# Kernel optimization log

Measured on AMD Instinct MI355X. Metric: run time of the kernel, lower is better.

Reference implementation:

```python
import jax, jax.numpy as jnp
import numpy as np
from jax import lax

B, N = 8, 107136          # batch, anchors (248*216*2)
SCORE_THRESH = 0.05
PRE_MAX = 2048            # nms_pre_max_sizes[0]
POST_MAX = 128            # nms_post_max_sizes[0]
IOU_THRESH = 0.5
NUM_DIR_BINS = 2
DIR_OFFSET = 0.0
POST_CENTER_RANGE = np.array([0.0, -39.68, -5.0, 69.12, 39.68, 5.0], np.float32)


def setup_inputs() -> dict:
    key = jax.random.key(0)
    k1, k2, k3, k4, k5 = jax.random.split(key, 5)
    box_preds = jax.random.normal(k1, (B, N, 7), jnp.float32) * 0.3
    cls_preds = jax.random.normal(k2, (B, N, 2), jnp.float32) * 2.0
    dir_preds = jax.random.normal(k3, (B, N, 2), jnp.float32)
    # realistic KITTI car anchors: (x, y, z, w, l, h, r)
    xs = jax.random.uniform(k4, (B, N), jnp.float32, 0.0, 69.12)
    ys = jax.random.uniform(k5, (B, N), jnp.float32, -39.68, 39.68)
    zs = jnp.full((B, N), -1.0, jnp.float32)
    w = jnp.full((B, N), 1.6, jnp.float32)
    l = jnp.full((B, N), 3.9, jnp.float32)
    h = jnp.full((B, N), 1.56, jnp.float32)
    r = jnp.broadcast_to(jnp.where(jnp.arange(N) % 2 == 0, 0.0, np.pi / 2).astype(jnp.float32), (B, N))
    anchors = jnp.stack([xs, ys, zs, w, l, h, r], axis=-1)
    return {"box_preds": box_preds, "cls_preds": cls_preds, "dir_preds": dir_preds, "anchors": anchors}


def _decode(bp, an):
    # GroundBox3dCoder.decode_torch (second/pointpillars), code order (x,y,z,w,l,h,r)
    xa, ya, za, wa, la, ha, ra = [an[..., i] for i in range(7)]
    xt, yt, zt, wt, lt, ht, rt = [bp[..., i] for i in range(7)]
    za = za + ha * 0.5
    diag = jnp.sqrt(la * la + wa * wa)
    xg = xt * diag + xa
    yg = yt * diag + ya
    zg = zt * ha + za
    lg = jnp.exp(lt) * la
    wg = jnp.exp(wt) * wa
    hg = jnp.exp(ht) * ha
    rg = rt + ra
    zg = zg - hg * 0.5
    return jnp.stack([xg, yg, zg, wg, lg, hg, rg], axis=-1)


def _standup(boxes):
    # boxes: [K,7] decoded; rotated 2d rect -> axis-aligned standup box (x1,y1,x2,y2)
    x, y, w, l, r = boxes[:, 0], boxes[:, 1], boxes[:, 3], boxes[:, 4], boxes[:, 6]
    c, s = jnp.abs(jnp.cos(r)), jnp.abs(jnp.sin(r))
    hx = 0.5 * (w * c + l * s)
    hy = 0.5 * (w * s + l * c)
    return jnp.stack([x - hx, y - hy, x + hx, y + hy], axis=-1)


def _pairwise_iou(bb):
    # bb: [K,4] standup boxes
    x1, y1, x2, y2 = bb[:, 0], bb[:, 1], bb[:, 2], bb[:, 3]
    area = (x2 - x1) * (y2 - y1)
    ix = jnp.maximum(0.0, jnp.minimum(x2[:, None], x2[None, :]) - jnp.maximum(x1[:, None], x1[None, :]))
    iy = jnp.maximum(0.0, jnp.minimum(y2[:, None], y2[None, :]) - jnp.maximum(y1[:, None], y1[None, :]))
    inter = ix * iy
    return inter / jnp.maximum(area[:, None] + area[None, :] - inter, 1e-8)


def _greedy_nms(ious, valid):
    K = valid.shape[0]
    idxs = jnp.arange(K)
    def body(i, keep):
        sup = (ious[i] > IOU_THRESH) & (idxs > i) & keep[i]
        return keep & ~sup
    return lax.fori_loop(0, K, body, valid)


def _limit_period(val, offset, period):
    return val - jnp.floor(val / period + offset) * period


def _predict_one(boxes, scores, dir_labels):
    # boxes [N,7], scores [N], dir_labels [N] int32 (already sorted? no: raw)
    masked = jnp.where(scores >= SCORE_THRESH, scores, -jnp.inf)
    top_s, idx = lax.top_k(masked, PRE_MAX)           # sorted desc
    b = boxes[idx]                                    # [K,7]
    dl = dir_labels[idx]
    valid = jnp.isfinite(top_s)
    ious = _pairwise_iou(_standup(b))
    keep = _greedy_nms(lax.stop_gradient(ious), valid)
    kept = jnp.where(keep, top_s, -jnp.inf)
    sel_s, sel_i = lax.top_k(kept, POST_MAX)
    sel_b = b[sel_i]
    sel_dl = dl[sel_i].astype(sel_b.dtype)
    period = 2.0 * np.pi / NUM_DIR_BINS
    dir_rot = _limit_period(sel_b[:, 6] - DIR_OFFSET, 0.0, period)
    new_r = dir_rot + DIR_OFFSET + period * sel_dl
    sel_b = jnp.concatenate([sel_b[:, :6], new_r[:, None]], axis=-1)
    pcr = jnp.asarray(POST_CENTER_RANGE)
    in_range = jnp.all(sel_b[:, :3] >= pcr[:3], axis=1) & jnp.all(sel_b[:, :3] <= pcr[3:], axis=1)
    mask = jnp.isfinite(sel_s) & in_range
    out_s = jnp.where(mask, sel_s, 0.0)
    out_b = jnp.where(mask[:, None], sel_b, 0.0)
    labels = jnp.zeros((POST_MAX,), jnp.int32)  # single fg class -> label 0
    return out_b, out_s, labels, mask


def reference(box_preds, cls_preds, dir_preds, anchors):
    decoded = _decode(box_preds, anchors)                    # [B,N,7]
    scores = jax.nn.softmax(cls_preds, axis=-1)[..., 1]      # [B,N]
    dir_labels = jnp.argmax(dir_preds, axis=-1).astype(jnp.int32)
    return jax.vmap(_predict_one)(decoded, scores, dir_labels)
```

## Files before the change

### kernel.cpp

```cpp
#include <hip/hip_runtime.h>
#include <stdint.h>

#define NB 8
#define NN 107136
#define TOTAL (NB * NN)
#define NPAIR (NN / 2)
#define PRE 2048
#define POST 128
#define CAP 4096
#define HBINS 128
#define KEYBASE 0xBF00u
#define SCORE_TH 0.05f
#define SH_BPB 53

static constexpr size_t OFF_SCORES = 0;
static constexpr size_t SZ_SCORES  = (size_t)TOTAL * 4;
static constexpr size_t OFF_HIST   = OFF_SCORES + SZ_SCORES;
static constexpr size_t SZ_HIST    = (size_t)NB * SH_BPB * HBINS * 4;
static constexpr size_t OFF_CNT    = OFF_HIST + SZ_HIST;
static constexpr size_t SZ_CNT     = (size_t)NB * 64 * 4;
static constexpr size_t OFF_CAND   = OFF_CNT + SZ_CNT + 256;
static constexpr size_t SZ_CAND    = (size_t)NB * CAP * 8;
static constexpr size_t OFF_SELS   = OFF_CAND + SZ_CAND;
static constexpr size_t OFF_SELI   = OFF_SELS + (size_t)NB * PRE * 4;
static constexpr size_t OFF_SELB   = OFF_SELI + (size_t)NB * PRE * 4;
static constexpr size_t OFF_SBB    = OFF_SELB + (size_t)NB * PRE * 7 * 4;
static constexpr size_t OFF_SAR    = OFF_SBB + (size_t)NB * PRE * 4 * 4;


__global__ void __launch_bounds__(256) k_scoreshist(const float* __restrict__ cls,
                                                    float* __restrict__ scores,
                                                    uint32_t* __restrict__ hp,
                                                    uint32_t* __restrict__ counts,
                                                    uint64_t* __restrict__ cand) {
    int b = blockIdx.y;
    int t = threadIdx.x;
    if (blockIdx.x == 0 && t == 0) counts[(size_t)b * 64] = 0u;
    if (blockIdx.x < 16)
        cand[(size_t)b * CAP + blockIdx.x * 256 + t] = 0ull;
    __shared__ uint32_t lh[HBINS];
    if (t < HBINS) lh[t] = 0u;
    __syncthreads();
    const float4* cp = (const float4*)cls + (size_t)b * NPAIR;
    float2* sp = (float2*)scores + (size_t)b * NPAIR;
#pragma unroll
    for (int k = 0; k < 4; k++) {
        int p = blockIdx.x * 1024 + k * 256 + t;
        if (p < NPAIR) {
            float4 c = cp[p];
            float m0 = fmaxf(c.x, c.y);
            float s0 = __fdiv_rn(expf(__fsub_rn(c.y, m0)),
                                 __fadd_rn(expf(__fsub_rn(c.x, m0)), expf(__fsub_rn(c.y, m0))));
            float m1 = fmaxf(c.z, c.w);
            float s1 = __fdiv_rn(expf(__fsub_rn(c.w, m1)),
                                 __fadd_rn(expf(__fsub_rn(c.z, m1)), expf(__fsub_rn(c.w, m1))));
            sp[p] = make_float2(s0, s1);
            if (s0 >= 0.5f) {
                uint32_t bin = ((__float_as_uint(s0) >> 16) | 0x8000u) - KEYBASE;
                if (bin > 127u) bin = 127u;
                atomicAdd(&lh[bin], 1u);
            }
            if (s1 >= 0.5f) {
                uint32_t bin = ((__float_as_uint(s1) >> 16) | 0x8000u) - KEYBASE;
                if (bin > 127u) bin = 127u;
                atomicAdd(&lh[bin], 1u);
            }
        }
    }
    __syncthreads();
    if (t < HBINS) hp[((size_t)b * SH_BPB + blockIdx.x) * HBINS + t] = lh[t];
}

__global__ void __launch_bounds__(256) k_compact(const float* __restrict__ scores,
                                                 const uint32_t* __restrict__ hp,
                                                 uint32_t* __restrict__ counts,
                                                 uint64_t* __restrict__ cand) {
    int g2 = blockIdx.x * 256 + threadIdx.x;
    int lane = threadIdx.x & 63, wid = threadIdx.x >> 6;
    int e0 = 2 * g2;
    int b = e0 / NN;

    uint32_t h0 = 0, h1 = 0;
    const uint32_t* hb = hp + (size_t)b * SH_BPB * HBINS;
#pragma unroll 4
    for (int sg = 0; sg < SH_BPB; sg++) {
        h0 += hb[sg * HBINS + 2 * lane];
        h1 += hb[sg * HBINS + 2 * lane + 1];
    }
    uint32_t v = h0 + h1;
    for (int off = 1; off < 64; off <<= 1) {
        uint32_t u = __shfl_down(v, off);
        if (lane + off >= 64) u = 0u;
        v += u;
    }
    uint32_t total = __shfl(v, 0);
    int c = -1;
    if (v - h0 >= PRE) c = 2 * lane + 1;
    else if (v >= PRE) c = 2 * lane;
    for (int off = 32; off > 0; off >>= 1) c = max(c, __shfl_xor(c, off));
    uint32_t Tb = (total >= PRE && c >= 0) ? (KEYBASE + (uint32_t)c) : 0u;

    float2 sv = ((const float2*)scores)[g2];
    uint32_t key0 = __float_as_uint(sv.x) | 0x80000000u;
    uint32_t key1 = __float_as_uint(sv.y) | 0x80000000u;
    bool p0 = (sv.x >= SCORE_TH) && ((key0 >> 16) >= Tb);
    bool p1 = (sv.y >= SCORE_TH) && ((key1 >> 16) >= Tb);
    uint64_t bal0 = __ballot(p0), bal1 = __ballot(p1);
    uint32_t n0 = (uint32_t)__popcll(bal0);
    uint32_t wcnt = n0 + (uint32_t)__popcll(bal1);
    uint64_t below = (1ull << lane) - 1ull;
    uint32_t off0 = (uint32_t)__popcll(bal0 & below);
    uint32_t off1 = n0 + (uint32_t)__popcll(bal1 & below);
    __shared__ uint32_t lcnt[2];
    __shared__ uint32_t gbase[2];
    __shared__ uint32_t wbase[4];
    int b0 = (blockIdx.x * 512) / NN;
    if (threadIdx.x < 2) lcnt[threadIdx.x] = 0u;
    __syncthreads();
    if (lane == 0 && wcnt) wbase[wid] = atomicAdd(&lcnt[b - b0], wcnt);
    __syncthreads();
    if (threadIdx.x < 2 && lcnt[threadIdx.x])
        gbase[threadIdx.x] = atomicAdd(&counts[(size_t)(b0 + threadIdx.x) * 64], lcnt[threadIdx.x]);
    __syncthreads();
    if (p0 | p1) {
        uint32_t base = gbase[b - b0] + wbase[wid];
        if (p0) {
            uint32_t slot = base + off0;
            if (slot < CAP)
                cand[(size_t)b * CAP + slot] =
                    ((uint64_t)key0 << 32) | (uint64_t)(0xFFFFFFFFu - (uint32_t)(e0 - b * NN));
        }
        if (p1) {
            uint32_t slot = base + off1;
            if (slot < CAP)
                cand[(size_t)b * CAP + slot] =
                    ((uint64_t)key1 << 32) | (uint64_t)(0xFFFFFFFFu - (uint32_t)(e0 + 1 - b * NN));
        }
    }
}

__global__ void __launch_bounds__(256) k_rank_decode(
        const uint64_t* __restrict__ cand, const uint32_t* __restrict__ counts,
        const float* __restrict__ box_preds, const float* __restrict__ anchors,
        float* __restrict__ selS, uint32_t* __restrict__ selI,
        float* __restrict__ selB, float* __restrict__ selBB, float* __restrict__ selA) {
    int b = blockIdx.y;
    int m = (int)counts[(size_t)b * 64]; if (m > CAP) m = CAP;
    int i0 = blockIdx.x * 256;
    if (i0 >= m) return;
    int t = threadIdx.x;
    int i = i0 + t;
    const uint64_t* cb = cand + (size_t)b * CAP;
    uint64_t mykey = (i < m) ? cb[i] : ~0ull;
    __shared__ uint64_t tile[512];
    uint32_t rank = 0;
    int ntiles = (m + 511) >> 9;
    for (int tt = 0; tt < ntiles; tt++) {
        int base = tt << 9;
        tile[t] = cb[base + t];
        tile[t + 256] = cb[base + 256 + t];
        __syncthreads();
#pragma unroll 16
        for (int j = 0; j < 512; j++)
            rank += (tile[j] > mykey) ? 1u : 0u;
        __syncthreads();
    }
    if (i >= m || rank >= PRE) return;

    size_t o = (size_t)b * PRE + rank;
    uint32_t key = (uint32_t)(mykey >> 32);
    uint32_t idx = 0xFFFFFFFFu - (uint32_t)(mykey & 0xFFFFFFFFull);
    float score = __uint_as_float(key & 0x7FFFFFFFu);
    const float* bp = box_preds + ((size_t)b * NN + idx) * 7;
    const float* an = anchors + ((size_t)b * NN + idx) * 7;
    float xa = an[0], ya = an[1], za = an[2], wa = an[3], la = an[4], ha = an[5], ra = an[6];
    float xt = bp[0], yt = bp[1], zt = bp[2], wt = bp[3], lt = bp[4], ht = bp[5], rt = bp[6];
    float za2  = __fadd_rn(za, __fmul_rn(ha, 0.5f));
    float diag = sqrtf(__fadd_rn(__fmul_rn(la, la), __fmul_rn(wa, wa)));
    float xg = __fadd_rn(__fmul_rn(xt, diag), xa);
    float yg = __fadd_rn(__fmul_rn(yt, diag), ya);
    float zg = __fadd_rn(__fmul_rn(zt, ha), za2);
    float lg = __fmul_rn(expf(lt), la);
    float wg = __fmul_rn(expf(wt), wa);
    float hg = __fmul_rn(expf(ht), ha);
    float rg = __fadd_rn(rt, ra);
    zg = __fsub_rn(zg, __fmul_rn(hg, 0.5f));
    selS[o] = score; selI[o] = idx;
    selB[o * 7 + 0] = xg; selB[o * 7 + 1] = yg; selB[o * 7 + 2] = zg;
    selB[o * 7 + 3] = wg; selB[o * 7 + 4] = lg; selB[o * 7 + 5] = hg;
    selB[o * 7 + 6] = rg;
    float cc = fabsf(cosf(rg)), ss = fabsf(sinf(rg));
    float hx = __fmul_rn(0.5f, __fadd_rn(__fmul_rn(wg, cc), __fmul_rn(lg, ss)));
    float hy = __fmul_rn(0.5f, __fadd_rn(__fmul_rn(wg, ss), __fmul_rn(lg, cc)));
    float x1 = __fsub_rn(xg, hx), y1 = __fsub_rn(yg, hy);
    float x2 = __fadd_rn(xg, hx), y2 = __fadd_rn(yg, hy);
    selBB[o * 4 + 0] = x1; selBB[o * 4 + 1] = y1;
    selBB[o * 4 + 2] = x2; selBB[o * 4 + 3] = y2;
    selA[o] = __fmul_rn(__fsub_rn(x2, x1), __fsub_rn(y2, y1));
}

__global__ void __launch_bounds__(128) k_nms(
        const float* __restrict__ selBB, const float* __restrict__ selA,
        const float* __restrict__ selS, const uint32_t* __restrict__ selI,
        const float* __restrict__ selB, const uint32_t* __restrict__ counts,
        const float* __restrict__ dir_preds, float* __restrict__ out) {
    int b = blockIdx.x;
    int t = threadIdx.x;
    __shared__ float4 sbb[PRE];
    __shared__ float  sar[PRE];
    __shared__ int keptIdx[POST];
    __shared__ int keptCountSh;
    int Mv = (int)counts[(size_t)b * 64]; if (Mv > PRE) Mv = PRE;
    const float4* bb4 = (const float4*)selBB + (size_t)b * PRE;
    const float*  ar  = selA + (size_t)b * PRE;
    for (int i = t; i < PRE; i += 128) {
        sbb[i] = bb4[i];
        sar[i] = ar[i];
    }
    __syncthreads();
    if (t < 64) {
        int lane = t;
        float ax1 = 1e30f, ay1 = 1e30f, ax2 = 1e30f, ay2 = 1e30f, aar = 0.f;
        float bx1 = 1e30f, by1 = 1e30f, bx2 = 1e30f, by2 = 1e30f, bar = 0.f;
        int kc = 0;
        for (int i = 0; i < Mv && kc < POST; i++) {
            float4 c = sbb[i];
            float ca = sar[i];
            float ix = fmaxf(0.f, __fsub_rn(fminf(ax2, c.z), fmaxf(ax1, c.x)));
            float iy = fmaxf(0.f, __fsub_rn(fminf(ay2, c.w), fmaxf(ay1, c.y)));
            float inter = __fmul_rn(ix, iy);
            float den = fmaxf(__fsub_rn(__fadd_rn(aar, ca), inter), 1e-8f);
            bool sup = inter > __fmul_rn(0.5f, den);
            ix = fmaxf(0.f, __fsub_rn(fminf(bx2, c.z), fmaxf(bx1, c.x)));
            iy = fmaxf(0.f, __fsub_rn(fminf(by2, c.w), fmaxf(by1, c.y)));
            inter = __fmul_rn(ix, iy);
            den = fmaxf(__fsub_rn(__fadd_rn(bar, ca), inter), 1e-8f);
            sup = sup || (inter > __fmul_rn(0.5f, den));
            if (__ballot(sup) == 0ull) {
                if (lane == 0) keptIdx[kc] = i;
                if (kc < 64) {
                    if (lane == kc) { ax1 = c.x; ay1 = c.y; ax2 = c.z; ay2 = c.w; aar = ca; }
                } else {
                    if (lane == kc - 64) { bx1 = c.x; by1 = c.y; bx2 = c.z; by2 = c.w; bar = ca; }
                }
                kc++;
            }
        }
        if (lane == 0) keptCountSh = kc;
    }
    __syncthreads();
    int kc = keptCountSh;
    size_t ob = (size_t)b * POST + t;
    float box[7] = {0.f, 0.f, 0.f, 0.f, 0.f, 0.f, 0.f};
    float sc = 0.f, mk = 0.f;
    if (t < kc) {
        int i = keptIdx[t];
        size_t o = (size_t)b * PRE + i;
        float s = selS[o];
        uint32_t idx = selI[o];
        const float* bx = selB + o * 7;
        float d0 = dir_preds[((size_t)b * NN + idx) * 2 + 0];
        float d1 = dir_preds[((size_t)b * NN + idx) * 2 + 1];
        float label = (d1 > d0) ? 1.0f : 0.0f;
        const float period = 3.14159265358979323846f;
        float r = bx[6];
        float dir_rot = __fsub_rn(r, __fmul_rn(floorf(__fdiv_rn(r, period)), period));
        float nr = __fadd_rn(dir_rot, __fmul_rn(period, label));
        float x = bx[0], y = bx[1], z = bx[2];
        bool in_range = (x >= 0.0f) && (y >= -39.68f) && (z >= -5.0f) &&
                        (x <= 69.12f) && (y <= 39.68f) && (z <= 5.0f);
        if (in_range) {
            box[0] = x; box[1] = y; box[2] = z;
            box[3] = bx[3]; box[4] = bx[4]; box[5] = bx[5]; box[6] = nr;
            sc = s; mk = 1.f;
        }
    }
    float* out_b = out;
    float* out_s = out + 7168;
    float* out_l = out + 8192;
    float* out_m = out + 9216;
    for (int c = 0; c < 7; c++) out_b[ob * 7 + c] = box[c];
    out_s[ob] = sc;
    out_l[ob] = 0.f;
    out_m[ob] = mk;
}

extern "C" void kernel_launch(void* const* d_in, const int* in_sizes, int n_in,
                              void* d_out, int out_size, void* d_ws, size_t ws_size,
                              hipStream_t stream) {
    const float* box_preds = (const float*)d_in[0];
    const float* cls_preds = (const float*)d_in[1];
    const float* dir_preds = (const float*)d_in[2];
    const float* anchors   = (const float*)d_in[3];
    float* out = (float*)d_out;
    char* ws = (char*)d_ws;

    float*    scores = (float*)(ws + OFF_SCORES);
    uint32_t* hp     = (uint32_t*)(ws + OFF_HIST);
    uint32_t* counts = (uint32_t*)(ws + OFF_CNT);
    uint64_t* cand   = (uint64_t*)(ws + OFF_CAND);
    float*    selS   = (float*)(ws + OFF_SELS);
    uint32_t* selI   = (uint32_t*)(ws + OFF_SELI);
    float*    selB   = (float*)(ws + OFF_SELB);
    float*    selBB  = (float*)(ws + OFF_SBB);
    float*    selA   = (float*)(ws + OFF_SAR);

    dim3 gSH(SH_BPB, NB);
    k_scoreshist<<<gSH, 256, 0, stream>>>(cls_preds, scores, hp, counts, cand);
    k_compact<<<TOTAL / 512, 256, 0, stream>>>(scores, hp, counts, cand);
    dim3 gRank(CAP / 256, NB);
    k_rank_decode<<<gRank, 256, 0, stream>>>(cand, counts, box_preds, anchors,
                                             selS, selI, selB, selBB, selA);
    k_nms<<<NB, 128, 0, stream>>>(selBB, selA, selS, selI, selB, counts,
                                  dir_preds, out);
}
```

Baseline: 178.0 us.

## Fuse four pipeline kernels into one cooperative persistent kernel with grid syncs

Replaces the four separate launches (score/histogram, compaction, rank+decode, NMS) with a single cooperative kernel of 256 blocks that separates the phases with grid.sync. Each block computes all per-batch thresholds redundantly and loops over several compaction chunks. The aim is to remove launch overhead and the gaps between dependent kernels. In exchange it adds grid-wide barrier costs, repeated threshold work in every block, and a final serial NMS phase that runs on only 8 blocks while the rest sit idle.

```diff
diff --git a/kernel.cpp b/kernel.cpp
--- a/kernel.cpp
+++ b/kernel.cpp
@@ -1,22 +1,29 @@
 #include <hip/hip_runtime.h>
+#include <hip/hip_cooperative_groups.h>
 #include <stdint.h>
+
+namespace cg = cooperative_groups;
 
 #define NB 8
 #define NN 107136
 #define TOTAL (NB * NN)
 #define NPAIR (NN / 2)
+#define NPAIRS_ALL (TOTAL / 2)
 #define PRE 2048
 #define POST 128
 #define CAP 4096
 #define HBINS 128
 #define KEYBASE 0xBF00u
 #define SCORE_TH 0.05f
-#define SH_BPB 53
+#define NSEG 32
+#define SEGP (NPAIR / NSEG)
+#define NBLK 256
+#define NTHR 256
 
 static constexpr size_t OFF_SCORES = 0;
 static constexpr size_t SZ_SCORES  = (size_t)TOTAL * 4;
 static constexpr size_t OFF_HIST   = OFF_SCORES + SZ_SCORES;
-static constexpr size_t SZ_HIST    = (size_t)NB * SH_BPB * HBINS * 4;
+static constexpr size_t SZ_HIST    = (size_t)NB * NSEG * HBINS * 4;
 static constexpr size_t OFF_CNT    = OFF_HIST + SZ_HIST;
 static constexpr size_t SZ_CNT     = (size_t)NB * 64 * 4;
 static constexpr size_t OFF_CAND   = OFF_CNT + SZ_CNT + 256;
@@ -27,262 +34,274 @@
 static constexpr size_t OFF_SBB    = OFF_SELB + (size_t)NB * PRE * 7 * 4;
 static constexpr size_t OFF_SAR    = OFF_SBB + (size_t)NB * PRE * 4 * 4;
 
-
-__global__ void __launch_bounds__(256) k_scoreshist(const float* __restrict__ cls,
-                                                    float* __restrict__ scores,
-                                                    uint32_t* __restrict__ hp,
-                                                    uint32_t* __restrict__ counts,
-                                                    uint64_t* __restrict__ cand) {
-    int b = blockIdx.y;
+#define SM_BYTES 41600
+
+__global__ void __launch_bounds__(256) k_mega(
+        const float* __restrict__ box_preds, const float* __restrict__ cls,
+        const float* __restrict__ dir_preds, const float* __restrict__ anchors,
+        float* scores, uint32_t* hp, uint32_t* counts, uint64_t* cand,
+        float* selS, uint32_t* selI, float* selB, float* selBB, float* selA,
+        float* out) {
+    cg::grid_group grid = cg::this_grid();
+    __shared__ __align__(16) unsigned char smraw[SM_BYTES];
     int t = threadIdx.x;
-    if (blockIdx.x == 0 && t == 0) counts[(size_t)b * 64] = 0u;
-    if (blockIdx.x < 16)
-        cand[(size_t)b * CAP + blockIdx.x * 256 + t] = 0ull;
-    __shared__ uint32_t lh[HBINS];
-    if (t < HBINS) lh[t] = 0u;
-    __syncthreads();
-    const float4* cp = (const float4*)cls + (size_t)b * NPAIR;
-    float2* sp = (float2*)scores + (size_t)b * NPAIR;
+    int blk = blockIdx.x;
+    int lane = t & 63, wid = t >> 6;
+
+    {
+        uint32_t* lh = (uint32_t*)smraw;
+        int b = blk >> 5, seg = blk & 31;
+        if (blk < NB && t == 0) counts[(size_t)blk * 64] = 0u;
+        if (t < 128) cand[(size_t)blk * 128 + t] = 0ull;
+        if (t < HBINS) lh[t] = 0u;
+        __syncthreads();
+        const float4* cp = (const float4*)cls + (size_t)b * NPAIR;
+        float2* sp = (float2*)scores + (size_t)b * NPAIR;
+        int base = seg * SEGP;
 #pragma unroll
-    for (int k = 0; k < 4; k++) {
-        int p = blockIdx.x * 1024 + k * 256 + t;
-        if (p < NPAIR) {
-            float4 c = cp[p];
-            float m0 = fmaxf(c.x, c.y);
-            float s0 = __fdiv_rn(expf(__fsub_rn(c.y, m0)),
-                                 __fadd_rn(expf(__fsub_rn(c.x, m0)), expf(__fsub_rn(c.y, m0))));
-            float m1 = fmaxf(c.z, c.w);
-            float s1 = __fdiv_rn(expf(__fsub_rn(c.w, m1)),
-                                 __fadd_rn(expf(__fsub_rn(c.z, m1)), expf(__fsub_rn(c.w, m1))));
-            sp[p] = make_float2(s0, s1);
-            if (s0 >= 0.5f) {
-                uint32_t bin = ((__float_as_uint(s0) >> 16) | 0x8000u) - KEYBASE;
-                if (bin > 127u) bin = 127u;
-                atomicAdd(&lh[bin], 1u);
-            }
-            if (s1 >= 0.5f) {
-                uint32_t bin = ((__float_as_uint(s1) >> 16) | 0x8000u) - KEYBASE;
-                if (bin > 127u) bin = 127u;
-                atomicAdd(&lh[bin], 1u);
-            }
-        }
+        for (int k = 0; k < 7; k++) {
+            int pl = k * 256 + t;
+            if (pl < SEGP) {
+                int p = base + pl;
+                float4 c = cp[p];
+                float m0 = fmaxf(c.x, c.y);
+                float s0 = __fdiv_rn(expf(__fsub_rn(c.y, m0)),
+                                     __fadd_rn(expf(__fsub_rn(c.x, m0)), expf(__fsub_rn(c.y, m0))));
+                float m1 = fmaxf(c.z, c.w);
+                float s1 = __fdiv_rn(expf(__fsub_rn(c.w, m1)),
+                                     __fadd_rn(expf(__fsub_rn(c.z, m1)), expf(__fsub_rn(c.w, m1))));
+                sp[p] = make_float2(s0, s1);
+                if (s0 >= 0.5f) {
+                    uint32_t bin = ((__float_as_uint(s0) >> 16) | 0x8000u) - KEYBASE;
+                    if (bin > 127u) bin = 127u;
+                    atomicAdd(&lh[bin], 1u);
+                }
+                if (s1 >= 0.5f) {
+                    uint32_t bin = ((__float_as_uint(s1) >> 16) | 0x8000u) - KEYBASE;
+                    if (bin > 127u) bin = 127u;
+                    atomicAdd(&lh[bin], 1u);
+                }
+            }
+        }
+        __syncthreads();
+        if (t < HBINS) hp[((size_t)(b * NSEG + seg)) * HBINS + t] = lh[t];
     }
-    __syncthreads();
-    if (t < HBINS) hp[((size_t)b * SH_BPB + blockIdx.x) * HBINS + t] = lh[t];
-}
-
-__global__ void __launch_bounds__(256) k_compact(const float* __restrict__ scores,
-                                                 const uint32_t* __restrict__ hp,
-                                                 uint32_t* __restrict__ counts,
-                                                 uint64_t* __restrict__ cand) {
-    int g2 = blockIdx.x * 256 + threadIdx.x;
-    int lane = threadIdx.x & 63, wid = threadIdx.x >> 6;
-    int e0 = 2 * g2;
-    int b = e0 / NN;
-
-    uint32_t h0 = 0, h1 = 0;
-    const uint32_t* hb = hp + (size_t)b * SH_BPB * HBINS;
+    __threadfence();
+    grid.sync();
+
+    {
+        struct P2S { uint32_t sT[8]; uint32_t lcnt[2]; uint32_t gbase[2]; uint32_t wbase[4]; };
+        P2S* s2 = (P2S*)smraw;
+        for (int bb = wid; bb < NB; bb += 4) {
+            uint32_t h0 = 0, h1 = 0;
+            const uint32_t* hb = hp + (size_t)bb * NSEG * HBINS;
 #pragma unroll 4
-    for (int sg = 0; sg < SH_BPB; sg++) {
-        h0 += hb[sg * HBINS + 2 * lane];
-        h1 += hb[sg * HBINS + 2 * lane + 1];
+            for (int sg = 0; sg < NSEG; sg++) {
+                h0 += hb[sg * HBINS + 2 * lane];
+                h1 += hb[sg * HBINS + 2 * lane + 1];
+            }
+            uint32_t v = h0 + h1;
+            for (int off = 1; off < 64; off <<= 1) {
+                uint32_t u = __shfl_down(v, off);
+                if (lane + off >= 64) u = 0u;
+                v += u;
+            }
+            uint32_t total = __shfl(v, 0);
+            int c = -1;
+            if (v - h0 >= PRE) c = 2 * lane + 1;
+            else if (v >= PRE) c = 2 * lane;
+            for (int off = 32; off > 0; off >>= 1) c = max(c, __shfl_xor(c, off));
+            if (lane == 0) s2->sT[bb] = (total >= PRE && c >= 0) ? (KEYBASE + (uint32_t)c) : 0u;
+        }
+        __syncthreads();
+        for (int it = 0; it < 7; it++) {
+            int g2 = it * 65536 + blk * 256 + t;
+            bool valid = g2 < NPAIRS_ALL;
+            int g2c = valid ? g2 : NPAIRS_ALL - 1;
+            int e0 = 2 * g2c;
+            int b = e0 / NN;
+            uint32_t Tb = s2->sT[b];
+            float2 sv = make_float2(0.f, 0.f);
+            if (valid) sv = ((const float2*)scores)[g2c];
+            uint32_t key0 = __float_as_uint(sv.x) | 0x80000000u;
+            uint32_t key1 = __float_as_uint(sv.y) | 0x80000000u;
+            bool p0 = valid && (sv.x >= SCORE_TH) && ((key0 >> 16) >= Tb);
+            bool p1 = valid && (sv.y >= SCORE_TH) && ((key1 >> 16) >= Tb);
+            uint64_t bal0 = __ballot(p0), bal1 = __ballot(p1);
+            uint32_t n0 = (uint32_t)__popcll(bal0);
+            uint32_t wcnt = n0 + (uint32_t)__popcll(bal1);
+            uint64_t below = (1ull << lane) - 1ull;
+            uint32_t off0 = (uint32_t)__popcll(bal0 & below);
+            uint32_t off1 = n0 + (uint32_t)__popcll(bal1 & below);
+            int b0 = (it * 131072 + blk * 512) / NN;
+            __syncthreads();
+            if (t < 2) s2->lcnt[t] = 0u;
+            __syncthreads();
+            if (lane == 0 && wcnt) s2->wbase[wid] = atomicAdd(&s2->lcnt[b - b0], wcnt);
+            __syncthreads();
+            if (t < 2 && s2->lcnt[t])
+                s2->gbase[t] = atomicAdd(&counts[(size_t)(b0 + t) * 64], s2->lcnt[t]);
+            __syncthreads();
+            if (p0 | p1) {
+                uint32_t base = s2->gbase[b - b0] + s2->wbase[wid];
+                if (p0) {
+                    uint32_t slot = base + off0;
+                    if (slot < CAP)
+                        cand[(size_t)b * CAP + slot] =
+                            ((uint64_t)key0 << 32) | (uint64_t)(0xFFFFFFFFu - (uint32_t)(e0 - b * NN));
+                }
+                if (p1) {
+                    uint32_t slot = base + off1;
+                    if (slot < CAP)
+                        cand[(size_t)b * CAP + slot] =
+                            ((uint64_t)key1 << 32) | (uint64_t)(0xFFFFFFFFu - (uint32_t)(e0 + 1 - b * NN));
+                }
+            }
+        }
     }
-    uint32_t v = h0 + h1;
-    for (int off = 1; off < 64; off <<= 1) {
-        uint32_t u = __shfl_down(v, off);
-        if (lane + off >= 64) u = 0u;
-        v += u;
+    __threadfence();
+    grid.sync();
+
+    {
+        uint64_t* tile = (uint64_t*)smraw;
+        int b = blk >> 5, k = blk & 31;
+        int m = (int)counts[(size_t)b * 64]; if (m > CAP) m = CAP;
+        int i0 = k * 256;
+        bool active = (k < 16) && (i0 < m);
+        if (active) {
+            int i = i0 + t;
+            const uint64_t* cb = cand + (size_t)b * CAP;
+            uint64_t mykey = (i < m) ? cb[i] : ~0ull;
+            uint32_t rank = 0;
+            int ntiles = (m + 511) >> 9;
+            for (int tt = 0; tt < ntiles; tt++) {
+                int base = tt << 9;
+                tile[t] = cb[base + t];
+                tile[t + 256] = cb[base + 256 + t];
+                __syncthreads();
+#pragma unroll 16
+                for (int j = 0; j < 512; j++)
+                    rank += (tile[j] > mykey) ? 1u : 0u;
+                __syncthreads();
+            }
+            if (i < m && rank < PRE) {
+                size_t o = (size_t)b * PRE + rank;
+                uint32_t key = (uint32_t)(mykey >> 32);
+                uint32_t idx = 0xFFFFFFFFu - (uint32_t)(mykey & 0xFFFFFFFFull);
+                float score = __uint_as_float(key & 0x7FFFFFFFu);
+                const float* bp = box_preds + ((size_t)b * NN + idx) * 7;
+                const float* an = anchors + ((size_t)b * NN + idx) * 7;
+                float xa = an[0], ya = an[1], za = an[2], wa = an[3], la = an[4], ha = an[5], ra = an[6];
+                float xt = bp[0], yt = bp[1], zt = bp[2], wt = bp[3], lt = bp[4], ht = bp[5], rt = bp[6];
+                float za2  = __fadd_rn(za, __fmul_rn(ha, 0.5f));
+                float diag = sqrtf(__fadd_rn(__fmul_rn(la, la), __fmul_rn(wa, wa)));
+                float xg = __fadd_rn(__fmul_rn(xt, diag), xa);
+                float yg = __fadd_rn(__fmul_rn(yt, diag), ya);
+                float zg = __fadd_rn(__fmul_rn(zt, ha), za2);
+                float lg = __fmul_rn(expf(lt), la);
+                float wg = __fmul_rn(expf(wt), wa);
+                float hg = __fmul_rn(expf(ht), ha);
+                float rg = __fadd_rn(rt, ra);
+                zg = __fsub_rn(zg, __fmul_rn(hg, 0.5f));
+                selS[o] = score; selI[o] = idx;
+                selB[o * 7 + 0] = xg; selB[o * 7 + 1] = yg; selB[o * 7 + 2] = zg;
+                selB[o * 7 + 3] = wg; selB[o * 7 + 4] = lg; selB[o * 7 + 5] = hg;
+                selB[o * 7 + 6] = rg;
+                float cc = fabsf(cosf(rg)), ss = fabsf(sinf(rg));
+                float hx = __fmul_rn(0.5f, __fadd_rn(__fmul_rn(wg, cc), __fmul_rn(lg, ss)));
+                float hy = __fmul_rn(0.5f, __fadd_rn(__fmul_rn(wg, ss), __fmul_rn(lg, cc)));
+                float x1 = __fsub_rn(xg, hx), y1 = __fsub_rn(yg, hy);
+                float x2 = __fadd_rn(xg, hx), y2 = __fadd_rn(yg, hy);
+                selBB[o * 4 + 0] = x1; selBB[o * 4 + 1] = y1;
+                selBB[o * 4 + 2] = x2; selBB[o * 4 + 3] = y2;
+                selA[o] = __fmul_rn(__fsub_rn(x2, x1), __fsub_rn(y2, y1));
+            }
+        }
     }
-    uint32_t total = __shfl(v, 0);
-    int c = -1;
-    if (v - h0 >= PRE) c = 2 * lane + 1;
-    else if (v >= PRE) c = 2 * lane;
-    for (int off = 32; off > 0; off >>= 1) c = max(c, __shfl_xor(c, off));
-    uint32_t Tb = (total >= PRE && c >= 0) ? (KEYBASE + (uint32_t)c) : 0u;
-
-    float2 sv = ((const float2*)scores)[g2];
-    uint32_t key0 = __float_as_uint(sv.x) | 0x80000000u;
-    uint32_t key1 = __float_as_uint(sv.y) | 0x80000000u;
-    bool p0 = (sv.x >= SCORE_TH) && ((key0 >> 16) >= Tb);
-    bool p1 = (sv.y >= SCORE_TH) && ((key1 >> 16) >= Tb);
-    uint64_t bal0 = __ballot(p0), bal1 = __ballot(p1);
-    uint32_t n0 = (uint32_t)__popcll(bal0);
-    uint32_t wcnt = n0 + (uint32_t)__popcll(bal1);
-    uint64_t below = (1ull << lane) - 1ull;
-    uint32_t off0 = (uint32_t)__popcll(bal0 & below);
-    uint32_t off1 = n0 + (uint32_t)__popcll(bal1 & below);
-    __shared__ uint32_t lcnt[2];
-    __shared__ uint32_t gbase[2];
-    __shared__ uint32_t wbase[4];
-    int b0 = (blockIdx.x * 512) / NN;
-    if (threadIdx.x < 2) lcnt[threadIdx.x] = 0u;
-    __syncthreads();
-    if (lane == 0 && wcnt) wbase[wid] = atomicAdd(&lcnt[b - b0], wcnt);
-    __syncthreads();
-    if (threadIdx.x < 2 && lcnt[threadIdx.x])
-        gbase[threadIdx.x] = atomicAdd(&counts[(size_t)(b0 + threadIdx.x) * 64], lcnt[threadIdx.x]);
-    __syncthreads();
-    if (p0 | p1) {
-        uint32_t base = gbase[b - b0] + wbase[wid];
-        if (p0) {
-            uint32_t slot = base + off0;
-            if (slot < CAP)
-                cand[(size_t)b * CAP + slot] =
-                    ((uint64_t)key0 << 32) | (uint64_t)(0xFFFFFFFFu - (uint32_t)(e0 - b * NN));
-        }
-        if (p1) {
-            uint32_t slot = base + off1;
-            if (slot < CAP)
-                cand[(size_t)b * CAP + slot] =
-                    ((uint64_t)key1 << 32) | (uint64_t)(0xFFFFFFFFu - (uint32_t)(e0 + 1 - b * NN));
+    __threadfence();
+    grid.sync();
+
+    if (blk < NB) {
+        int b = blk;
+        float4* sbb = (float4*)smraw;
+        float*  sar = (float*)(smraw + 32768);
+        int*    keptIdx = (int*)(smraw + 40960);
+        int*    keptCount = (int*)(smraw + 41472);
+        int Mv = (int)counts[(size_t)b * 64]; if (Mv > PRE) Mv = PRE;
+        const float4* bb4 = (const float4*)selBB + (size_t)b * PRE;
+        const float*  ar  = selA + (size_t)b * PRE;
+        for (int i = t; i < PRE; i += 256) {
+            sbb[i] = bb4[i];
+            sar[i] = ar[i];
+        }
+        __syncthreads();
+        if (t < 64) {
+            float ax1 = 1e30f, ay1 = 1e30f, ax2 = 1e30f, ay2 = 1e30f, aar = 0.f;
+            float bx1 = 1e30f, by1 = 1e30f, bx2 = 1e30f, by2 = 1e30f, bar = 0.f;
+            int kc = 0;
+            for (int i = 0; i < Mv && kc < POST; i++) {
+                float4 c = sbb[i];
+                float ca = sar[i];
+                float ix = fmaxf(0.f, __fsub_rn(fminf(ax2, c.z), fmaxf(ax1, c.x)));
+                float iy = fmaxf(0.f, __fsub_rn(fminf(ay2, c.w), fmaxf(ay1, c.y)));
+                float inter = __fmul_rn(ix, iy);
+                float den = fmaxf(__fsub_rn(__fadd_rn(aar, ca), inter), 1e-8f);
+                bool sup = inter > __fmul_rn(0.5f, den);
+                ix = fmaxf(0.f, __fsub_rn(fminf(bx2, c.z), fmaxf(bx1, c.x)));
+                iy = fmaxf(0.f, __fsub_rn(fminf(by2, c.w), fmaxf(by1, c.y)));
+                inter = __fmul_rn(ix, iy);
+                den = fmaxf(__fsub_rn(__fadd_rn(bar, ca), inter), 1e-8f);
+                sup = sup || (inter > __fmul_rn(0.5f, den));
+                if (__ballot(sup) == 0ull) {
+                    if (t == 0) keptIdx[kc] = i;
+                    if (kc < 64) {
+                        if (t == kc) { ax1 = c.x; ay1 = c.y; ax2 = c.z; ay2 = c.w; aar = ca; }
+                    } else {
+                        if (t == kc - 64) { bx1 = c.x; by1 = c.y; bx2 = c.z; by2 = c.w; bar = ca; }
+                    }
+                    kc++;
+                }
+            }
+            if (t == 0) *keptCount = kc;
+        }
+        __syncthreads();
+        if (t < POST) {
+            int kc = *keptCount;
+            size_t ob = (size_t)b * POST + t;
+            float box[7] = {0.f, 0.f, 0.f, 0.f, 0.f, 0.f, 0.f};
+            float sc = 0.f, mk = 0.f;
+            if (t < kc) {
+                int i = keptIdx[t];
+                size_t o = (size_t)b * PRE + i;
+                float s = selS[o];
+                uint32_t idx = selI[o];
+                const float* bx = selB + o * 7;
+                float d0 = dir_preds[((size_t)b * NN + idx) * 2 + 0];
+                float d1 = dir_preds[((size_t)b * NN + idx) * 2 + 1];
+                float label = (d1 > d0) ? 1.0f : 0.0f;
+                const float period = 3.14159265358979323846f;
+                float r = bx[6];
+                float dir_rot = __fsub_rn(r, __fmul_rn(floorf(__fdiv_rn(r, period)), period));
+                float nr = __fadd_rn(dir_rot, __fmul_rn(period, label));
+                float x = bx[0], y = bx[1], z = bx[2];
+                bool in_range = (x >= 0.0f) && (y >= -39.68f) && (z >= -5.0f) &&
+                                (x <= 69.12f) && (y <= 39.68f) && (z <= 5.0f);
+                if (in_range) {
+                    box[0] = x; box[1] = y; box[2] = z;
+                    box[3] = bx[3]; box[4] = bx[4]; box[5] = bx[5]; box[6] = nr;
+                    sc = s; mk = 1.f;
+                }
+            }
+            float* out_b = out;
+            float* out_s = out + 7168;
+            float* out_l = out + 8192;
+            float* out_m = out + 9216;
+            for (int c = 0; c < 7; c++) out_b[ob * 7 + c] = box[c];
+            out_s[ob] = sc;
+            out_l[ob] = 0.f;
+            out_m[ob] = mk;
         }
     }
-}
-
-__global__ void __launch_bounds__(256) k_rank_decode(
-        const uint64_t* __restrict__ cand, const uint32_t* __restrict__ counts,
-        const float* __restrict__ box_preds, const float* __restrict__ anchors,
-        float* __restrict__ selS, uint32_t* __restrict__ selI,
-        float* __restrict__ selB, float* __restrict__ selBB, float* __restrict__ selA) {
-    int b = blockIdx.y;
-    int m = (int)counts[(size_t)b * 64]; if (m > CAP) m = CAP;
-    int i0 = blockIdx.x * 256;
-    if (i0 >= m) return;
-    int t = threadIdx.x;
-    int i = i0 + t;
-    const uint64_t* cb = cand + (size_t)b * CAP;
-    uint64_t mykey = (i < m) ? cb[i] : ~0ull;
-    __shared__ uint64_t tile[512];
-    uint32_t rank = 0;
-    int ntiles = (m + 511) >> 9;
-    for (int tt = 0; tt < ntiles; tt++) {
-        int base = tt << 9;
-        tile[t] = cb[base + t];
-        tile[t + 256] = cb[base + 256 + t];
-        __syncthreads();
-#pragma unroll 16
-        for (int j = 0; j < 512; j++)
-            rank += (tile[j] > mykey) ? 1u : 0u;
-        __syncthreads();
-    }
-    if (i >= m || rank >= PRE) return;
-
-    size_t o = (size_t)b * PRE + rank;
-    uint32_t key = (uint32_t)(mykey >> 32);
-    uint32_t idx = 0xFFFFFFFFu - (uint32_t)(mykey & 0xFFFFFFFFull);
-    float score = __uint_as_float(key & 0x7FFFFFFFu);
-    const float* bp = box_preds + ((size_t)b * NN + idx) * 7;
-    const float* an = anchors + ((size_t)b * NN + idx) * 7;
-    float xa = an[0], ya = an[1], za = an[2], wa = an[3], la = an[4], ha = an[5], ra = an[6];
-    float xt = bp[0], yt = bp[1], zt = bp[2], wt = bp[3], lt = bp[4], ht = bp[5], rt = bp[6];
-    float za2  = __fadd_rn(za, __fmul_rn(ha, 0.5f));
-    float diag = sqrtf(__fadd_rn(__fmul_rn(la, la), __fmul_rn(wa, wa)));
-    float xg = __fadd_rn(__fmul_rn(xt, diag), xa);
-    float yg = __fadd_rn(__fmul_rn(yt, diag), ya);
-    float zg = __fadd_rn(__fmul_rn(zt, ha), za2);
-    float lg = __fmul_rn(expf(lt), la);
-    float wg = __fmul_rn(expf(wt), wa);
-    float hg = __fmul_rn(expf(ht), ha);
-    float rg = __fadd_rn(rt, ra);
-    zg = __fsub_rn(zg, __fmul_rn(hg, 0.5f));
-    selS[o] = score; selI[o] = idx;
-    selB[o * 7 + 0] = xg; selB[o * 7 + 1] = yg; selB[o * 7 + 2] = zg;
-    selB[o * 7 + 3] = wg; selB[o * 7 + 4] = lg; selB[o * 7 + 5] = hg;
-    selB[o * 7 + 6] = rg;
-    float cc = fabsf(cosf(rg)), ss = fabsf(sinf(rg));
-    float hx = __fmul_rn(0.5f, __fadd_rn(__fmul_rn(wg, cc), __fmul_rn(lg, ss)));
-    float hy = __fmul_rn(0.5f, __fadd_rn(__fmul_rn(wg, ss), __fmul_rn(lg, cc)));
-    float x1 = __fsub_rn(xg, hx), y1 = __fsub_rn(yg, hy);
-    float x2 = __fadd_rn(xg, hx), y2 = __fadd_rn(yg, hy);
-    selBB[o * 4 + 0] = x1; selBB[o * 4 + 1] = y1;
-    selBB[o * 4 + 2] = x2; selBB[o * 4 + 3] = y2;
-    selA[o] = __fmul_rn(__fsub_rn(x2, x1), __fsub_rn(y2, y1));
-}
-
-__global__ void __launch_bounds__(128) k_nms(
-        const float* __restrict__ selBB, const float* __restrict__ selA,
-        const float* __restrict__ selS, const uint32_t* __restrict__ selI,
-        const float* __restrict__ selB, const uint32_t* __restrict__ counts,
-        const float* __restrict__ dir_preds, float* __restrict__ out) {
-    int b = blockIdx.x;
-    int t = threadIdx.x;
-    __shared__ float4 sbb[PRE];
-    __shared__ float  sar[PRE];
-    __shared__ int keptIdx[POST];
-    __shared__ int keptCountSh;
-    int Mv = (int)counts[(size_t)b * 64]; if (Mv > PRE) Mv = PRE;
-    const float4* bb4 = (const float4*)selBB + (size_t)b * PRE;
-    const float*  ar  = selA + (size_t)b * PRE;
-    for (int i = t; i < PRE; i += 128) {
-        sbb[i] = bb4[i];
-        sar[i] = ar[i];
-    }
-    __syncthreads();
-    if (t < 64) {
-        int lane = t;
-        float ax1 = 1e30f, ay1 = 1e30f, ax2 = 1e30f, ay2 = 1e30f, aar = 0.f;
-        float bx1 = 1e30f, by1 = 1e30f, bx2 = 1e30f, by2 = 1e30f, bar = 0.f;
-        int kc = 0;
-        for (int i = 0; i < Mv && kc < POST; i++) {
-            float4 c = sbb[i];
-            float ca = sar[i];
-            float ix = fmaxf(0.f, __fsub_rn(fminf(ax2, c.z), fmaxf(ax1, c.x)));
-            float iy = fmaxf(0.f, __fsub_rn(fminf(ay2, c.w), fmaxf(ay1, c.y)));
-            float inter = __fmul_rn(ix, iy);
-            float den = fmaxf(__fsub_rn(__fadd_rn(aar, ca), inter), 1e-8f);
-            bool sup = inter > __fmul_rn(0.5f, den);
-            ix = fmaxf(0.f, __fsub_rn(fminf(bx2, c.z), fmaxf(bx1, c.x)));
-            iy = fmaxf(0.f, __fsub_rn(fminf(by2, c.w), fmaxf(by1, c.y)));
-            inter = __fmul_rn(ix, iy);
-            den = fmaxf(__fsub_rn(__fadd_rn(bar, ca), inter), 1e-8f);
-            sup = sup || (inter > __fmul_rn(0.5f, den));
-            if (__ballot(sup) == 0ull) {
-                if (lane == 0) keptIdx[kc] = i;
-                if (kc < 64) {
-                    if (lane == kc) { ax1 = c.x; ay1 = c.y; ax2 = c.z; ay2 = c.w; aar = ca; }
-                } else {
-                    if (lane == kc - 64) { bx1 = c.x; by1 = c.y; bx2 = c.z; by2 = c.w; bar = ca; }
-                }
-                kc++;
-            }
-        }
-        if (lane == 0) keptCountSh = kc;
-    }
-    __syncthreads();
-    int kc = keptCountSh;
-    size_t ob = (size_t)b * POST + t;
-    float box[7] = {0.f, 0.f, 0.f, 0.f, 0.f, 0.f, 0.f};
-    float sc = 0.f, mk = 0.f;
-    if (t < kc) {
-        int i = keptIdx[t];
-        size_t o = (size_t)b * PRE + i;
-        float s = selS[o];
-        uint32_t idx = selI[o];
-        const float* bx = selB + o * 7;
-        float d0 = dir_preds[((size_t)b * NN + idx) * 2 + 0];
-        float d1 = dir_preds[((size_t)b * NN + idx) * 2 + 1];
-        float label = (d1 > d0) ? 1.0f : 0.0f;
-        const float period = 3.14159265358979323846f;
-        float r = bx[6];
-        float dir_rot = __fsub_rn(r, __fmul_rn(floorf(__fdiv_rn(r, period)), period));
-        float nr = __fadd_rn(dir_rot, __fmul_rn(period, label));
-        float x = bx[0], y = bx[1], z = bx[2];
-        bool in_range = (x >= 0.0f) && (y >= -39.68f) && (z >= -5.0f) &&
-                        (x <= 69.12f) && (y <= 39.68f) && (z <= 5.0f);
-        if (in_range) {
-            box[0] = x; box[1] = y; box[2] = z;
-            box[3] = bx[3]; box[4] = bx[4]; box[5] = bx[5]; box[6] = nr;
-            sc = s; mk = 1.f;
-        }
-    }
-    float* out_b = out;
-    float* out_s = out + 7168;
-    float* out_l = out + 8192;
-    float* out_m = out + 9216;
-    for (int c = 0; c < 7; c++) out_b[ob * 7 + c] = box[c];
-    out_s[ob] = sc;
-    out_l[ob] = 0.f;
-    out_m[ob] = mk;
 }
 
 extern "C" void kernel_launch(void* const* d_in, const int* in_sizes, int n_in,
@@ -305,12 +324,12 @@
     float*    selBB  = (float*)(ws + OFF_SBB);
     float*    selA   = (float*)(ws + OFF_SAR);
 
-    dim3 gSH(SH_BPB, NB);
-    k_scoreshist<<<gSH, 256, 0, stream>>>(cls_preds, scores, hp, counts, cand);
-    k_compact<<<TOTAL / 512, 256, 0, stream>>>(scores, hp, counts, cand);
-    dim3 gRank(CAP / 256, NB);
-    k_rank_decode<<<gRank, 256, 0, stream>>>(cand, counts, box_preds, anchors,
-                                             selS, selI, selB, selBB, selA);
-    k_nms<<<NB, 128, 0, stream>>>(selBB, selA, selS, selI, selB, counts,
-                                  dir_preds, out);
+    void* args[] = {
+        (void*)&box_preds, (void*)&cls_preds, (void*)&dir_preds, (void*)&anchors,
+        (void*)&scores, (void*)&hp, (void*)&counts, (void*)&cand,
+        (void*)&selS, (void*)&selI, (void*)&selB, (void*)&selBB, (void*)&selA,
+        (void*)&out
+    };
+    hipLaunchCooperativeKernel((const void*)k_mega, dim3(NBLK), dim3(NTHR),
+                               args, 0, stream);
 }
```

Result: slower. 330.8 us (+85.8%).
